# Kernel optimization log

Hardware: AMD Instinct MI355X
Metric: run time of the kernel (lower is better)

Reference implementation:

```python
import jax, jax.numpy as jnp
import numpy as np
import math

EPS = 1e-6
P_MIN = 1e-3
P_MAX = 10.0
NUM_ITERS = 3
REG = 1.0
K = 64       # num_clusters
D = 128      # cluster_dim
TOKEN = 256  # token_dim
B, N, C = 8, 8192, 512


def _l2norm(t):
    return t / jnp.clip(jnp.linalg.norm(t, axis=-1, keepdims=True), 1e-12)


def _mlp(h, W1, b1, W2, b2):
    # torch Linear: y = h @ W.T + b ; dropout is identity at eval
    return jax.nn.relu(h @ W1.T + b1) @ W2.T + b2


def _log_otp_solver(log_a, log_b, M, num_iters, reg):
    M = M / reg
    u = jnp.zeros_like(log_a)
    v = jnp.zeros_like(log_b)
    for _ in range(num_iters):  # fixed small iteration count
        u = log_a - jax.scipy.special.logsumexp(M + v[:, None, :], axis=2)
        v = log_b - jax.scipy.special.logsumexp(M + u[:, :, None], axis=1)
    return M + u[:, :, None] + v[:, None, :]


def _get_matching_probs(S, dustbin_score, num_iters, reg):
    b, m, n = S.shape
    dust_row = jnp.broadcast_to(dustbin_score, (b, 1, n)).astype(S.dtype)
    S_aug = jnp.concatenate([S, dust_row], axis=1)  # [b, m+1, n]
    norm = -math.log(n + m)
    log_a = jnp.full((m + 1,), norm, dtype=S.dtype).at[-1].add(math.log(n - m))
    log_a = jnp.broadcast_to(log_a, (b, m + 1))
    log_b = jnp.full((b, n), norm, dtype=S.dtype)
    log_P = _log_otp_solver(log_a, log_b, S_aug, num_iters, reg)
    return log_P - norm


def setup_inputs() -> dict:
    key = jax.random.key(0)
    ks = jax.random.split(key, 8)
    x = jax.random.normal(ks[0], (B, N, C), dtype=jnp.float32)

    def lin(k, fin, fout):
        k1, k2 = jax.random.split(k)
        W = 0.02 * jax.random.normal(k1, (fout, fin), dtype=jnp.float32)
        b = 0.02 * jax.random.normal(k2, (fout,), dtype=jnp.float32)
        return W, b

    tW1, tb1 = lin(ks[1], C, 512)
    tW2, tb2 = lin(ks[2], 512, TOKEN)
    cW1, cb1 = lin(ks[3], C, 512)
    cW2, cb2 = lin(ks[4], 512, D)
    sW1, sb1 = lin(ks[5], C, 512)
    sW2, sb2 = lin(ks[6], 512, K)
    # GeM p param init so that softplus(w)+p_min == 3.0
    gem_w = jnp.array([math.log(math.exp(3.0 - P_MIN) - 1.0)], dtype=jnp.float32)
    dust_bin = jnp.array(1.0, dtype=jnp.float32)
    return dict(x=x, gem_w=gem_w, dust_bin=dust_bin,
                tW1=tW1, tb1=tb1, tW2=tW2, tb2=tb2,
                cW1=cW1, cb1=cb1, cW2=cW2, cb2=cb2,
                sW1=sW1, sb1=sb1, sW2=sW2, sb2=sb2)


def reference(x, gem_w, dust_bin,
              tW1, tb1, tW2, tb2,
              cW1, cb1, cW2, cb2,
              sW1, sb1, sW2, sb2):
    # --- GeM pooling: [B, N, C] -> [B, C] ---
    p = jnp.minimum(jax.nn.softplus(gem_w) + P_MIN, P_MAX)  # [1]
    g = jnp.mean(jnp.clip(x.astype(jnp.float32), EPS, None) ** p, axis=1) ** (1.0 / p)
    g = jnp.where(jnp.isfinite(g), g, jnp.zeros_like(g))

    global_token = _mlp(g, tW1, tb1, tW2, tb2)          # [B, TOKEN]
    local = _mlp(x, cW1, cb1, cW2, cb2)                 # [B, N, D]
    scores = _mlp(x, sW1, sb1, sW2, sb2)                # [B, N, K]

    S = scores.transpose(0, 2, 1)                       # [B, K, N]
    log_P = _get_matching_probs(S, dust_bin, NUM_ITERS, REG)  # [B, K+1, N]
    p_mat = jnp.exp(log_P)[:, :-1, :]                   # drop dustbin -> [B, K, N]

    # aggregated[b, d, k] = sum_n local[b, n, d] * p[b, k, n]  (no O(B*D*K*N) blowup)
    agg = jnp.einsum('bnd,bkn->bdk', local, p_mat).reshape(x.shape[0], -1)  # [B, D*K]

    result = jnp.concatenate([_l2norm(global_token), _l2norm(agg)], axis=-1)
    return _l2norm(result)
```

## Files before the change

kernel.cpp:

```cpp
#include <hip/hip_runtime.h>
#include <hip/hip_bf16.h>
#include <math.h>

#define BB   8
#define NN   8192
#define CC   512
#define DD   128
#define KK   64
#define TOK  256
#define MM   (BB*NN)

typedef unsigned short u16;
typedef __attribute__((ext_vector_type(8))) short short8;
typedef __attribute__((ext_vector_type(4))) float floatx4;

struct PtrSz { const void* p[15]; int sz[15]; };

__device__ __forceinline__ float bf2f(u16 v) {
    union { unsigned u; float f; } x; x.u = ((unsigned)v) << 16; return x.f;
}
__device__ __forceinline__ u16 f2bf(float f) {
    union { float f; unsigned u; } x; x.f = f;
    unsigned r = x.u + 0x7fffu + ((x.u >> 16) & 1u);
    return (u16)(r >> 16);
}
__device__ __forceinline__ float nat_exp2(float a) {
    float r; asm("v_exp_f32 %0, %1" : "=v"(r) : "v"(a)); return r;
}
__device__ __forceinline__ float nat_log2(float a) {
    float r; asm("v_log_f32 %0, %1" : "=v"(r) : "v"(a)); return r;
}
__device__ __forceinline__ void gload16(const void* g, void* l) {
    __builtin_amdgcn_global_load_lds(
        (const __attribute__((address_space(1))) void*)g,
        (__attribute__((address_space(3))) void*)l, 16, 0, 0);
}

__global__ __launch_bounds__(256)
void fill_sentinel(float* __restrict__ out, int n, float val) {
    int i = blockIdx.x*256 + threadIdx.x;
    if (i < n) out[i] = val;
}

__global__ __launch_bounds__(256)
void detect_all(PtrSz ps, int* __restrict__ flags) {
    int i = blockIdx.x;
    const u16* q = (const u16*)ps.p[i];
    int m = ps.sz[i] < 4096 ? ps.sz[i] : 4096;
    __shared__ int cnt;
    if (threadIdx.x == 0) cnt = 0;
    __syncthreads();
    int c = 0;
    for (int j = threadIdx.x; j < m; j += 256) {
        int e = (q[j] >> 7) & 0xFF;
        if (e < 90 || e > 165) c++;
    }
    atomicAdd(&cnt, c);
    __syncthreads();
    if (threadIdx.x == 0) flags[i] = (cnt * 8 > m) ? 1 : 0;
}

#define W_TW1 0
#define W_TB1 262144
#define W_TW2 262656
#define W_TB2 393728
#define W_CW1 393984
#define W_CB1 656128
#define W_CW2 656640
#define W_CB2 722176
#define W_SW1 722304
#define W_SB1 984448
#define W_SW2 984960
#define W_SB2 1017728
#define W_TOTAL 1017792

__global__ __launch_bounds__(256)
void conv_weights(PtrSz ps, const int* __restrict__ flags,
                  u16* __restrict__ wbuf, float* __restrict__ wscal) {
    long gid = (long)blockIdx.x*256 + threadIdx.x;
    if (gid == 0) {
        float vb = bf2f(((const u16*)ps.p[1])[0]);
        float vf = ((const float*)ps.p[1])[0];
        wscal[0] = (fabsf(vb - 2.94694f) < 0.2f) ? vb : vf;
    } else if (gid == 1) {
        float vb = bf2f(((const u16*)ps.p[2])[0]);
        float vf = ((const float*)ps.p[2])[0];
        wscal[1] = (fabsf(vb - 1.0f) < 0.2f) ? vb : vf;
    }
    if (gid >= W_TOTAL) return;
    int idx; long off;
    if      (gid < W_TB1) { idx = 3;  off = W_TW1; }
    else if (gid < W_TW2) { idx = 4;  off = W_TB1; }
    else if (gid < W_TB2) { idx = 5;  off = W_TW2; }
    else if (gid < W_CW1) { idx = 6;  off = W_TB2; }
    else if (gid < W_CB1) { idx = 7;  off = W_CW1; }
    else if (gid < W_CW2) { idx = 8;  off = W_CB1; }
    else if (gid < W_CB2) { idx = 9;  off = W_CW2; }
    else if (gid < W_SW1) { idx = 10; off = W_CB2; }
    else if (gid < W_SB1) { idx = 11; off = W_SW1; }
    else if (gid < W_SW2) { idx = 12; off = W_SB1; }
    else if (gid < W_SB2) { idx = 13; off = W_SW2; }
    else                  { idx = 14; off = W_SB2; }
    long k = gid - off;
    bool f32in = flags[idx] != 0;
    wbuf[gid] = f32in ? f2bf(((const float*)ps.p[idx])[k]) : ((const u16*)ps.p[idx])[k];
}

__global__ __launch_bounds__(256)
void gem_partial(const void* __restrict__ x, const float* __restrict__ wscal,
                 const int* __restrict__ flags, float* __restrict__ gacc) {
    __shared__ float red[4][512];
    int b = blockIdx.x, ny = blockIdx.y;
    int tid  = threadIdx.x;
    int wave = tid >> 6, lane = tid & 63;
    bool f32in = (flags[0] != 0);
    float gw = wscal[0];
    float p  = fminf(log1pf(expf(gw)) + 1e-3f, 10.0f);
    int c0 = lane*8;
    float s[8];
#pragma unroll
    for (int j = 0; j < 8; ++j) s[j] = 0.f;
    size_t base = ((size_t)b*NN + (size_t)ny*64 + wave)*CC + c0;
    if (f32in) {
        const float* xf = (const float*)x;
#pragma unroll 4
        for (int n = 0; n < 64; n += 4) {
            const float* pf = xf + base + (size_t)n*CC;
            float4 x0 = *(const float4*)pf;
            float4 x1 = *(const float4*)(pf + 4);
            float xv[8] = {x0.x,x0.y,x0.z,x0.w,x1.x,x1.y,x1.z,x1.w};
#pragma unroll
            for (int j = 0; j < 8; ++j)
                s[j] += nat_exp2(p * nat_log2(fmaxf(xv[j], 1e-6f)));
        }
    } else {
        const u16* xu = (const u16*)x;
#pragma unroll 4
        for (int n = 0; n < 64; n += 4) {
            short8 v8 = *(const short8*)(xu + base + (size_t)n*CC);
#pragma unroll
            for (int j = 0; j < 8; ++j)
                s[j] += nat_exp2(p * nat_log2(fmaxf(bf2f((u16)v8[j]), 1e-6f)));
        }
    }
#pragma unroll
    for (int j = 0; j < 8; ++j) red[wave][c0 + j] = s[j];
    __syncthreads();
#pragma unroll
    for (int t = 0; t < 2; ++t) {
        int c = tid + t*256;
        float v = red[0][c] + red[1][c] + red[2][c] + red[3][c];
        atomicAdd(&gacc[b*CC + c], v);
    }
}

__global__ __launch_bounds__(256)
void gem_finalize(const float* __restrict__ gacc, const float* __restrict__ wscal,
                  float* __restrict__ g) {
    int i = blockIdx.x*256 + threadIdx.x;
    float gw = wscal[0];
    float p  = fminf(log1pf(expf(gw)) + 1e-3f, 10.0f);
    float m  = gacc[i] / (float)NN;
    float r  = powf(m, 1.0f/p);
    if (!isfinite(r)) r = 0.f;
    g[i] = r;
}

__global__ __launch_bounds__(512)
void token_mlp(const float* __restrict__ g, const u16* __restrict__ wbuf,
               float* __restrict__ t) {
    __shared__ float gs[CC];
    __shared__ float hs[512];
    int b = blockIdx.x, j = threadIdx.x;
    gs[j] = g[b*CC + j];
    __syncthreads();
    float a = bf2f(wbuf[W_TB1 + j]);
    const u16* w = wbuf + W_TW1 + (size_t)j*CC;
    for (int c = 0; c < CC; ++c) a += gs[c]*bf2f(w[c]);
    hs[j] = fmaxf(a, 0.f);
    __syncthreads();
    if (j < TOK) {
        float a2 = bf2f(wbuf[W_TB2 + j]);
        const u16* w2 = wbuf + W_TW2 + (size_t)j*512;
        for (int c = 0; c < 512; ++c) a2 += hs[c]*bf2f(w2[c]);
        t[b*TOK + j] = a2;
    }
}

template<int BN, int MODE, bool RELU, bool ARAW>
__global__ __launch_bounds__(256)
void gemm_bt(const void* __restrict__ A, const u16* __restrict__ W,
             const u16* __restrict__ bias, void* __restrict__ Cout,
             const int* __restrict__ flags, int N, int Ksz, int lda,
             size_t a_base, int bidx_ovr,
             const u16* __restrict__ W_alt, const u16* __restrict__ bias_alt,
             int nsplit) {
    constexpr int WSUB_N = BN/32;
    constexpr int ATILE = 128*32;
    constexpr int BTILE = BN*32;
    extern __shared__ char smem[];
    u16* a0 = (u16*)smem;
    u16* b0 = a0 + ATILE;
    u16* a1 = b0 + BTILE;
    u16* b1 = a1 + ATILE;
    const int tid  = threadIdx.x;
    const int wave = tid >> 6, lane = tid & 63;
    const int wm = wave >> 1, wn = wave & 1;

    int bx = blockIdx.x, by = blockIdx.y;
    {
        int nbx = gridDim.x, nby = gridDim.y;
        int nwg = nbx*nby;
        if ((nwg & 7) == 0) {
            int lid = bx + by*nbx;
            int q = nwg >> 3;
            int t = (lid & 7)*q + (lid >> 3);
            by = t % nby;
            bx = t / nby;
        }
    }
    const u16* Wp = W; const u16* bp = bias;
    int byw = by;
    if (W_alt != nullptr && by >= nsplit) { Wp = W_alt; bp = bias_alt; byw = by - nsplit; }
    const int bm0 = bx * 128;
    const int bn0 = by * BN;
    const int bw0 = byw * BN;
    const int fr = lane & 15;
    const int fk = (lane >> 4) * 8;
    const bool f32in = ARAW && (flags[0] != 0);

    floatx4 acc[4][WSUB_N];
#pragma unroll
    for (int i = 0; i < 4; ++i)
#pragma unroll
        for (int j = 0; j < WSUB_N; ++j) acc[i][j] = (floatx4){0.f,0.f,0.f,0.f};

    auto STAGE = [&](u16* ab, u16* bb, int k0) {
#pragma unroll
        for (int part = 0; part < 2; ++part) {
            int cb = part*256 + wave*64;
            int mych = cb + lane;
            int row = mych >> 2, kc = (mych & 3)*8;
            gload16((const u16*)A + a_base + (size_t)(bm0 + row)*lda + k0 + kc,
                    ab + (size_t)cb*8);
        }
#pragma unroll
        for (int part = 0; part < BN/64; ++part) {
            int cb = part*256 + wave*64;
            int mych = cb + lane;
            int row = mych >> 2, kc = (mych & 3)*8;
            gload16(Wp + (size_t)(bw0 + row)*Ksz + k0 + kc,
                    bb + (size_t)cb*8);
        }
    };
    auto COMPUTE = [&](const u16* ab, const u16* bb) {
        short8 af[4], bfr[WSUB_N];
#pragma unroll
        for (int i = 0; i < 4; ++i)
            af[i] = *(const short8*)(ab + (wm*64 + i*16 + fr)*32 + fk);
#pragma unroll
        for (int j = 0; j < WSUB_N; ++j)
            bfr[j] = *(const short8*)(bb + (wn*WSUB_N*16 + j*16 + fr)*32 + fk);
#pragma unroll
        for (int i = 0; i < 4; ++i)
#pragma unroll
            for (int j = 0; j < WSUB_N; ++j)
                acc[i][j] = __builtin_amdgcn_mfma_f32_16x16x32_bf16(af[i], bfr[j], acc[i][j], 0, 0, 0);
    };

    if (!f32in) {
        STAGE(a0, b0, 0);
        __syncthreads();
        for (int k0 = 0; k0 < Ksz; k0 += 64) {
            if (k0 + 32 < Ksz) STAGE(a1, b1, k0 + 32);
            COMPUTE(a0, b0);
            __syncthreads();
            if (k0 + 64 < Ksz) STAGE(a0, b0, k0 + 64);
            COMPUTE(a1, b1);
            __syncthreads();
        }
    } else {
        for (int k0 = 0; k0 < Ksz; k0 += 32) {
#pragma unroll
            for (int part = 0; part < 2; ++part) {
                int chunk = part*256 + tid;
                int row = chunk >> 2, kc = (chunk & 3)*8;
                size_t gidx = a_base + (size_t)(bm0 + row)*lda + k0 + kc;
                const float* pf = (const float*)A + gidx;
                float4 x0 = *(const float4*)pf;
                float4 x1 = *(const float4*)(pf + 4);
                short8 vA;
                vA[0]=(short)f2bf(x0.x); vA[1]=(short)f2bf(x0.y);
                vA[2]=(short)f2bf(x0.z); vA[3]=(short)f2bf(x0.w);
                vA[4]=(short)f2bf(x1.x); vA[5]=(short)f2bf(x1.y);
                vA[6]=(short)f2bf(x1.z); vA[7]=(short)f2bf(x1.w);
                *(short8*)(a0 + row*32 + kc) = vA;
            }
#pragma unroll
            for (int part = 0; part < BN/64; ++part) {
                int cb = part*256 + wave*64;
                int mych = cb + lane;
                int row = mych >> 2, kc = (mych & 3)*8;
                gload16(Wp + (size_t)(bw0 + row)*Ksz + k0 + kc,
                        b0 + (size_t)cb*8);
            }
            __syncthreads();
            COMPUTE(a0, b0);
            __syncthreads();
        }
    }

    if constexpr (MODE == 0) {
        u16* cs = (u16*)smem;
#pragma unroll
        for (int i = 0; i < 4; ++i) {
            int row0 = wm*64 + i*16 + ((lane>>4)<<2);
#pragma unroll
            for (int j = 0; j < WSUB_N; ++j) {
                int col = wn*WSUB_N*16 + j*16 + fr;
                float bb = bf2f(bp[bw0+col]);
#pragma unroll
                for (int r = 0; r < 4; ++r) {
                    float v = acc[i][j][r] + bb;
                    if (RELU) v = fmaxf(v, 0.f);
                    cs[(row0+r)*BN + col] = f2bf(v);
                }
            }
        }
        __syncthreads();
        u16* C = (u16*)Cout;
#pragma unroll
        for (int c = 0; c < (128*BN)/(256*8); ++c) {
            int flat = (c*256 + tid)*8;
            int rowt = flat / BN, colt = flat % BN;
            *(short8*)(C + (size_t)(bm0+rowt)*N + bn0 + colt) =
                *(const short8*)(cs + flat);
        }
    } else {
        const int bidx = (bidx_ovr >= 0) ? bidx_ovr : (bm0 >> 13);
        const int nin  = bm0 & 8191;
        if constexpr (MODE == 1) {
            u16* tr = (u16*)smem;
#pragma unroll
            for (int i = 0; i < 4; ++i) {
                int row0 = wm*64 + i*16 + ((lane>>4)<<2);
#pragma unroll
                for (int j = 0; j < WSUB_N; ++j) {
                    int col = wn*WSUB_N*16 + j*16 + fr;
                    float bb = bf2f(bp[bw0+col]);
#pragma unroll
                    for (int r = 0; r < 4; ++r) {
                        float v = acc[i][j][r] + bb;
                        if (RELU) v = fmaxf(v, 0.f);
                        tr[col*128 + row0 + r] = f2bf(v);
                    }
                }
            }
            __syncthreads();
            u16* O = (u16*)Cout;
#pragma unroll
            for (int c = 0; c < (BN*128)/256; ++c) {
                int flat = c*256 + tid;
                int dcol = flat >> 7, rr = flat & 127;
                O[(size_t)(bidx*BN + bn0 + dcol)*NN + nin + rr] = tr[dcol*128 + rr];
            }
        } else {
            float* tr = (float*)smem;
#pragma unroll
            for (int i = 0; i < 4; ++i) {
                int row0 = wm*64 + i*16 + ((lane>>4)<<2);
#pragma unroll
                for (int j = 0; j < WSUB_N; ++j) {
                    int col = wn*WSUB_N*16 + j*16 + fr;
                    float bb = bf2f(bp[bw0+col]);
#pragma unroll
                    for (int r = 0; r < 4; ++r) {
                        float v = acc[i][j][r] + bb;
                        if (RELU) v = fmaxf(v, 0.f);
                        tr[col*128 + row0 + r] = v;
                    }
                }
            }
            __syncthreads();
            float* O = (float*)Cout;
#pragma unroll
            for (int c = 0; c < (BN*128)/256; ++c) {
                int flat = c*256 + tid;
                int dcol = flat >> 7, rr = flat & 127;
                O[(size_t)(bidx*BN + bn0 + dcol)*NN + nin + rr] = tr[dcol*128 + rr];
            }
        }
    }
}

__global__ __launch_bounds__(256)
void sink_u(const float* __restrict__ ST, const float* __restrict__ v,
            const float* __restrict__ wscal, float* __restrict__ u) {
    int m = blockIdx.x, b = blockIdx.y, t = threadIdx.x;
    const float norm = -logf(8256.0f);
    float la = (m == 64) ? norm + logf(8128.0f) : norm;
    float dustf = wscal[1];
    const float* vb = v + (size_t)b*NN;
    float r[32];
    float mx = -1e30f;
    if (m < 64) {
        const float* row = ST + ((size_t)b*64 + m)*NN;
#pragma unroll
        for (int i = 0; i < 32; ++i) { int n = t + i*256; r[i] = row[n] + vb[n]; mx = fmaxf(mx, r[i]); }
    } else {
#pragma unroll
        for (int i = 0; i < 32; ++i) { int n = t + i*256; r[i] = dustf + vb[n]; mx = fmaxf(mx, r[i]); }
    }
#pragma unroll
    for (int off = 32; off; off >>= 1) mx = fmaxf(mx, __shfl_xor(mx, off));
    __shared__ float red[4];
    if ((t & 63) == 0) red[t>>6] = mx;
    __syncthreads();
    mx = fmaxf(fmaxf(red[0], red[1]), fmaxf(red[2], red[3]));
    __syncthreads();
    float s = 0.f;
#pragma unroll
    for (int i = 0; i < 32; ++i) s += expf(r[i] - mx);
#pragma unroll
    for (int off = 32; off; off >>= 1) s += __shfl_xor(s, off);
    if ((t & 63) == 0) red[t>>6] = s;
    __syncthreads();
    s = red[0] + red[1] + red[2] + red[3];
    if (t == 0) u[b*65 + m] = la - (mx + logf(s));
}

template<int WP>
__global__ __launch_bounds__(256)
void sink_v_t(const float* __restrict__ ST, const float* __restrict__ u,
              const float* __restrict__ wscal, float* __restrict__ v,
              u16* __restrict__ P) {
    int b = blockIdx.y;
    int n = blockIdx.x*256 + threadIdx.x;
    __shared__ float us[65];
    if (threadIdx.x < 65) us[threadIdx.x] = u[b*65 + threadIdx.x];
    __syncthreads();
    const float norm = -logf(8256.0f);
    float mx = wscal[1] + us[64];
    float s  = 1.0f;
    const float* col = ST + (size_t)b*64*NN + n;
    if (WP) {
        float r[64];
#pragma unroll
        for (int m = 0; m < 64; ++m) {
            r[m] = col[(size_t)m*NN] + us[m];
            float nm = fmaxf(mx, r[m]);
            s = s*expf(mx - nm) + expf(r[m] - nm);
            mx = nm;
        }
        float vn = norm - (mx + logf(s));
        v[(size_t)b*NN + n] = vn;
#pragma unroll
        for (int k = 0; k < 64; ++k)
            P[((size_t)b*64 + k)*NN + n] = f2bf(expf(r[k] + vn - norm));
    } else {
        for (int m = 0; m < 64; ++m) {
            float tv = col[(size_t)m*NN] + us[m];
            float nm = fmaxf(mx, tv);
            s = s*expf(mx - nm) + expf(tv - nm);
            mx = nm;
        }
        v[(size_t)b*NN + n] = norm - (mx + logf(s));
    }
}

__global__ __launch_bounds__(256)
void agg_mfma(const u16* __restrict__ localT, const u16* __restrict__ P,
              float* __restrict__ agg) {
    __shared__ u16 a_lds[128*32];
    __shared__ u16 b_lds[64*32];
    int b = blockIdx.y, ns = blockIdx.x;
    int n0 = ns*256;
    const int tid  = threadIdx.x;
    const int wave = tid >> 6, lane = tid & 63;
    const int wm = wave >> 1, wn = wave & 1;
    const int fr = lane & 15, fk = (lane >> 4)*8;

    floatx4 acc[4][2];
#pragma unroll
    for (int i = 0; i < 4; ++i)
#pragma unroll
        for (int j = 0; j < 2; ++j) acc[i][j] = (floatx4){0.f,0.f,0.f,0.f};

    for (int s = 0; s < 8; ++s) {
        int nk = n0 + s*32;
#pragma unroll
        for (int part = 0; part < 2; ++part) {
            int chunk = part*256 + tid;
            int row = chunk >> 2, kc = (chunk & 3)*8;
            short8 vA = *(const short8*)(localT + ((size_t)b*128 + row)*NN + nk + kc);
            *(short8*)(a_lds + row*32 + kc) = vA;
        }
        {
            int row = tid >> 2, kc = (tid & 3)*8;
            short8 vB = *(const short8*)(P + ((size_t)b*64 + row)*NN + nk + kc);
            *(short8*)(b_lds + row*32 + kc) = vB;
        }
        __syncthreads();
        short8 af[4], bfr[2];
#pragma unroll
        for (int i = 0; i < 4; ++i)
            af[i] = *(const short8*)(a_lds + (wm*64 + i*16 + fr)*32 + fk);
#pragma unroll
        for (int j = 0; j < 2; ++j)
            bfr[j] = *(const short8*)(b_lds + (wn*32 + j*16 + fr)*32 + fk);
#pragma unroll
        for (int i = 0; i < 4; ++i)
#pragma unroll
            for (int j = 0; j < 2; ++j)
                acc[i][j] = __builtin_amdgcn_mfma_f32_16x16x32_bf16(af[i], bfr[j], acc[i][j], 0, 0, 0);
        __syncthreads();
    }
#pragma unroll
    for (int i = 0; i < 4; ++i) {
        int d0 = wm*64 + i*16 + ((lane>>4)<<2);
#pragma unroll
        for (int j = 0; j < 2; ++j) {
            int k = wn*32 + j*16 + fr;
#pragma unroll
            for (int r = 0; r < 4; ++r)
                atomicAdd(&agg[(size_t)b*8192 + (d0+r)*64 + k], acc[i][j][r]);
        }
    }
}

__global__ __launch_bounds__(256)
void finalize_out(const float* __restrict__ tg, const float* __restrict__ agg,
                  float* __restrict__ out) {
    int b = blockIdx.x, tid = threadIdx.x;
    float tv = tg[b*TOK + tid];
    float s1 = tv*tv;
    const float* ab = agg + (size_t)b*8192;
    float av[32];
    float s2 = 0.f;
#pragma unroll
    for (int i = 0; i < 32; ++i) { av[i] = ab[tid + i*256]; s2 += av[i]*av[i]; }
#pragma unroll
    for (int off = 32; off; off >>= 1) { s1 += __shfl_xor(s1, off); s2 += __shfl_xor(s2, off); }
    __shared__ float r1[4], r2[4];
    int wave = tid >> 6, lane = tid & 63;
    if (lane == 0) { r1[wave] = s1; r2[wave] = s2; }
    __syncthreads();
    float S1 = r1[0]+r1[1]+r1[2]+r1[3];
    float S2 = r2[0]+r2[1]+r2[2]+r2[3];
    const float rs2 = 1.41421356237f;
    float sc1 = 1.0f/(fmaxf(sqrtf(S1), 1e-12f)*rs2);
    float sc2 = 1.0f/(fmaxf(sqrtf(S2), 1e-12f)*rs2);
    out[(size_t)b*8448 + tid] = tv*sc1;
#pragma unroll
    for (int i = 0; i < 32; ++i)
        out[(size_t)b*8448 + 256 + tid + i*256] = av[i]*sc2;
}

extern "C" void kernel_launch(void* const* d_in, const int* in_sizes, int n_in,
                              void* d_out, int out_size, void* d_ws, size_t ws_size,
                              hipStream_t stream) {
    float* out = (float*)d_out;

    static const int EXP[15] = {33554432,1,1,262144,512,131072,256,
                                262144,512,65536,128,262144,512,32768,64};
    bool ok = (n_in == 15) && (out_size == 67584);
    if (ok) for (int i = 0; i < 15; ++i) ok = ok && (in_sizes[i] == EXP[i]);
    if (!ok) {
        fill_sentinel<<<264, 256, 0, stream>>>(out, out_size, 0.25f);
        return;
    }
    const size_t NEED_BATCH = 52934656ull;
    if (ws_size < NEED_BATCH) {
        fill_sentinel<<<264, 256, 0, stream>>>(out, out_size, 0.5f);
        return;
    }

    const void* x = d_in[0];
    PtrSz ps;
    for (int i = 0; i < 15; ++i) { ps.p[i] = d_in[i]; ps.sz[i] = in_sizes[i]; }

    char* base = (char*)d_ws;
    float* gacc = (float*)(base + 0);
    float* u    = (float*)(base + 16384);
    float* v    = (float*)(base + 18464);
    float* agg  = (float*)(base + 280608);
    const size_t ZERO_BYTES = 542752;
    float* g    = (float*)(base + 542752);
    float* tglb = (float*)(base + 559136);
    int*   flags= (int*)  (base + 567328);
    float* wscal= (float*)(base + 567392);
    u16*   wbuf = (u16*)  (base + 567424);
    float* ST   = (float*)(base + 2603008);
    u16* localT = (u16*)  (base + 19380224);
    u16* P      = (u16*)  (base + 36157440);
    u16* h1     = (u16*)  (base + 44546048);
    const size_t FULL_NEED  = 44546048ull + 67108864ull;
    const size_t FUSED_NEED = 44546048ull + 134217728ull;
    const bool fused = (ws_size >= FUSED_NEED);
    const bool mono  = (ws_size >= FULL_NEED);

    hipMemsetAsync(d_ws, 0, ZERO_BYTES, stream);

    detect_all<<<15, 256, 0, stream>>>(ps, flags);
    conv_weights<<<3977, 256, 0, stream>>>(ps, flags, wbuf, wscal);

    gem_partial<<<dim3(BB, 128), 256, 0, stream>>>(x, wscal, flags, gacc);
    gem_finalize<<<16, 256, 0, stream>>>(gacc, wscal, g);
    token_mlp<<<BB, 512, 0, stream>>>(g, wbuf, tglb);

    const int NOSPLIT = 1 << 30;
    if (fused) {
        gemm_bt<128, 0, true,  true ><<<dim3(512, 8), 256, 32768, stream>>>(
            x, wbuf + W_CW1, wbuf + W_CB1, h1, flags, 1024, 512, 512, 0, -1,
            wbuf + W_SW1, wbuf + W_SB1, 4);
        gemm_bt<128, 1, false, false><<<dim3(512, 1), 256, 32768, stream>>>(
            h1, wbuf + W_CW2, wbuf + W_CB2, localT, flags, 128, 512, 1024, 0, -1,
            nullptr, nullptr, NOSPLIT);
        gemm_bt< 64, 2, false, false><<<dim3(512, 1), 256, 32768, stream>>>(
            h1, wbuf + W_SW2, wbuf + W_SB2, ST, flags, 64, 512, 1024, 512, -1,
            nullptr, nullptr, NOSPLIT);
    } else if (mono) {
        gemm_bt<128, 0, true,  true ><<<dim3(512, 4), 256, 32768, stream>>>(
            x, wbuf + W_CW1, wbuf + W_CB1, h1, flags, 512, 512, 512, 0, -1,
            nullptr, nullptr, NOSPLIT);
        gemm_bt<128, 1, false, false><<<dim3(512, 1), 256, 32768, stream>>>(
            h1, wbuf + W_CW2, wbuf + W_CB2, localT, flags, 128, 512, 512, 0, -1,
            nullptr, nullptr, NOSPLIT);
        gemm_bt<128, 0, true,  true ><<<dim3(512, 4), 256, 32768, stream>>>(
            x, wbuf + W_SW1, wbuf + W_SB1, h1, flags, 512, 512, 512, 0, -1,
            nullptr, nullptr, NOSPLIT);
        gemm_bt< 64, 2, false, false><<<dim3(512, 1), 256, 32768, stream>>>(
            h1, wbuf + W_SW2, wbuf + W_SB2, ST, flags, 64, 512, 512, 0, -1,
            nullptr, nullptr, NOSPLIT);
    } else {
        for (int b = 0; b < BB; ++b) {
            size_t ab = (size_t)b*NN*CC;
            gemm_bt<128, 0, true,  true ><<<dim3(64, 4), 256, 32768, stream>>>(
                x, wbuf + W_CW1, wbuf + W_CB1, h1, flags, 512, 512, 512, ab, -1,
                nullptr, nullptr, NOSPLIT);
            gemm_bt<128, 1, false, false><<<dim3(64, 1), 256, 32768, stream>>>(
                h1, wbuf + W_CW2, wbuf + W_CB2, localT, flags, 128, 512, 512, 0, b,
                nullptr, nullptr, NOSPLIT);
            gemm_bt<128, 0, true,  true ><<<dim3(64, 4), 256, 32768, stream>>>(
                x, wbuf + W_SW1, wbuf + W_SB1, h1, flags, 512, 512, 512, ab, -1,
                nullptr, nullptr, NOSPLIT);
            gemm_bt< 64, 2, false, false><<<dim3(64, 1), 256, 32768, stream>>>(
                h1, wbuf + W_SW2, wbuf + W_SB2, ST, flags, 64, 512, 512, 0, b,
                nullptr, nullptr, NOSPLIT);
        }
    }

    for (int it = 0; it < 3; ++it) {
        sink_u<<<dim3(65, BB), 256, 0, stream>>>(ST, v, wscal, u);
        if (it == 2)
            sink_v_t<1><<<dim3(32, BB), 256, 0, stream>>>(ST, u, wscal, v, P);
        else
            sink_v_t<0><<<dim3(32, BB), 256, 0, stream>>>(ST, u, wscal, v, P);
    }

    agg_mfma<<<dim3(32, BB), 256, 0, stream>>>(localT, P, agg);
    finalize_out<<<BB, 256, 0, stream>>>(tglb, agg, out);
}
```

Measured before the change: 547.1 us.

## Drop GEMM LDS double buffering and write MODE 0 output directly to global

Replaces the double-buffered LDS staging loop in gemm_bt with a single-buffered load/sync/compute/sync loop. The MODE 0 epilogue now writes scalar bf16 values straight to global memory instead of staging through LDS for vectorized 16-byte stores. The first-layer GEMM launches drop their dynamic shared memory request from 32 KB to 16 KB, which may allow more workgroups per CU. In exchange it loses the overlap of global loads with MFMA compute and replaces coalesced wide stores with scattered 2-byte writes.

```diff
diff --git a/kernel.cpp b/kernel.cpp
--- a/kernel.cpp
+++ b/kernel.cpp
@@ -196,13 +196,9 @@
              const u16* __restrict__ W_alt, const u16* __restrict__ bias_alt,
              int nsplit) {
     constexpr int WSUB_N = BN/32;
-    constexpr int ATILE = 128*32;
-    constexpr int BTILE = BN*32;
     extern __shared__ char smem[];
-    u16* a0 = (u16*)smem;
-    u16* b0 = a0 + ATILE;
-    u16* a1 = b0 + BTILE;
-    u16* b1 = a1 + ATILE;
+    u16* a_lds = (u16*)smem;
+    u16* b_lds = (u16*)smem + 128*32;
     const int tid  = threadIdx.x;
     const int wave = tid >> 6, lane = tid & 63;
     const int wm = wave >> 1, wn = wave & 1;
@@ -235,52 +231,8 @@
 #pragma unroll
         for (int j = 0; j < WSUB_N; ++j) acc[i][j] = (floatx4){0.f,0.f,0.f,0.f};
 
-    auto STAGE = [&](u16* ab, u16* bb, int k0) {
-#pragma unroll
-        for (int part = 0; part < 2; ++part) {
-            int cb = part*256 + wave*64;
-            int mych = cb + lane;
-            int row = mych >> 2, kc = (mych & 3)*8;
-            gload16((const u16*)A + a_base + (size_t)(bm0 + row)*lda + k0 + kc,
-                    ab + (size_t)cb*8);
-        }
-#pragma unroll
-        for (int part = 0; part < BN/64; ++part) {
-            int cb = part*256 + wave*64;
-            int mych = cb + lane;
-            int row = mych >> 2, kc = (mych & 3)*8;
-            gload16(Wp + (size_t)(bw0 + row)*Ksz + k0 + kc,
-                    bb + (size_t)cb*8);
-        }
-    };
-    auto COMPUTE = [&](const u16* ab, const u16* bb) {
-        short8 af[4], bfr[WSUB_N];
-#pragma unroll
-        for (int i = 0; i < 4; ++i)
-            af[i] = *(const short8*)(ab + (wm*64 + i*16 + fr)*32 + fk);
-#pragma unroll
-        for (int j = 0; j < WSUB_N; ++j)
-            bfr[j] = *(const short8*)(bb + (wn*WSUB_N*16 + j*16 + fr)*32 + fk);
-#pragma unroll
-        for (int i = 0; i < 4; ++i)
-#pragma unroll
-            for (int j = 0; j < WSUB_N; ++j)
-                acc[i][j] = __builtin_amdgcn_mfma_f32_16x16x32_bf16(af[i], bfr[j], acc[i][j], 0, 0, 0);
-    };
-
-    if (!f32in) {
-        STAGE(a0, b0, 0);
-        __syncthreads();
-        for (int k0 = 0; k0 < Ksz; k0 += 64) {
-            if (k0 + 32 < Ksz) STAGE(a1, b1, k0 + 32);
-            COMPUTE(a0, b0);
-            __syncthreads();
-            if (k0 + 64 < Ksz) STAGE(a0, b0, k0 + 64);
-            COMPUTE(a1, b1);
-            __syncthreads();
-        }
-    } else {
-        for (int k0 = 0; k0 < Ksz; k0 += 32) {
+    for (int k0 = 0; k0 < Ksz; k0 += 32) {
+        if (f32in) {
 #pragma unroll
             for (int part = 0; part < 2; ++part) {
                 int chunk = part*256 + tid;
@@ -294,24 +246,44 @@
                 vA[2]=(short)f2bf(x0.z); vA[3]=(short)f2bf(x0.w);
                 vA[4]=(short)f2bf(x1.x); vA[5]=(short)f2bf(x1.y);
                 vA[6]=(short)f2bf(x1.z); vA[7]=(short)f2bf(x1.w);
-                *(short8*)(a0 + row*32 + kc) = vA;
+                *(short8*)(a_lds + row*32 + kc) = vA;
             }
-#pragma unroll
-            for (int part = 0; part < BN/64; ++part) {
+        } else {
+#pragma unroll
+            for (int part = 0; part < 2; ++part) {
                 int cb = part*256 + wave*64;
                 int mych = cb + lane;
                 int row = mych >> 2, kc = (mych & 3)*8;
-                gload16(Wp + (size_t)(bw0 + row)*Ksz + k0 + kc,
-                        b0 + (size_t)cb*8);
+                gload16((const u16*)A + a_base + (size_t)(bm0 + row)*lda + k0 + kc,
+                        a_lds + (size_t)cb*8);
             }
-            __syncthreads();
-            COMPUTE(a0, b0);
-            __syncthreads();
-        }
+        }
+#pragma unroll
+        for (int part = 0; part < BN/64; ++part) {
+            int cb = part*256 + wave*64;
+            int mych = cb + lane;
+            int row = mych >> 2, kc = (mych & 3)*8;
+            gload16(Wp + (size_t)(bw0 + row)*Ksz + k0 + kc,
+                    b_lds + (size_t)cb*8);
+        }
+        __syncthreads();
+        short8 af[4], bfr[WSUB_N];
+#pragma unroll
+        for (int i = 0; i < 4; ++i)
+            af[i] = *(const short8*)(a_lds + (wm*64 + i*16 + fr)*32 + fk);
+#pragma unroll
+        for (int j = 0; j < WSUB_N; ++j)
+            bfr[j] = *(const short8*)(b_lds + (wn*WSUB_N*16 + j*16 + fr)*32 + fk);
+#pragma unroll
+        for (int i = 0; i < 4; ++i)
+#pragma unroll
+            for (int j = 0; j < WSUB_N; ++j)
+                acc[i][j] = __builtin_amdgcn_mfma_f32_16x16x32_bf16(af[i], bfr[j], acc[i][j], 0, 0, 0);
+        __syncthreads();
     }
 
     if constexpr (MODE == 0) {
-        u16* cs = (u16*)smem;
+        u16* C = (u16*)Cout;
 #pragma unroll
         for (int i = 0; i < 4; ++i) {
             int row0 = wm*64 + i*16 + ((lane>>4)<<2);
@@ -323,18 +295,9 @@
                 for (int r = 0; r < 4; ++r) {
                     float v = acc[i][j][r] + bb;
                     if (RELU) v = fmaxf(v, 0.f);
-                    cs[(row0+r)*BN + col] = f2bf(v);
+                    C[(size_t)(bm0+row0+r)*N + (bn0+col)] = f2bf(v);
                 }
             }
-        }
-        __syncthreads();
-        u16* C = (u16*)Cout;
-#pragma unroll
-        for (int c = 0; c < (128*BN)/(256*8); ++c) {
-            int flat = (c*256 + tid)*8;
-            int rowt = flat / BN, colt = flat % BN;
-            *(short8*)(C + (size_t)(bm0+rowt)*N + bn0 + colt) =
-                *(const short8*)(cs + flat);
         }
     } else {
         const int bidx = (bidx_ovr >= 0) ? bidx_ovr : (bm0 >> 13);
@@ -610,7 +573,7 @@
 
     const int NOSPLIT = 1 << 30;
     if (fused) {
-        gemm_bt<128, 0, true,  true ><<<dim3(512, 8), 256, 32768, stream>>>(
+        gemm_bt<128, 0, true,  true ><<<dim3(512, 8), 256, 16384, stream>>>(
             x, wbuf + W_CW1, wbuf + W_CB1, h1, flags, 1024, 512, 512, 0, -1,
             wbuf + W_SW1, wbuf + W_SB1, 4);
         gemm_bt<128, 1, false, false><<<dim3(512, 1), 256, 32768, stream>>>(
@@ -620,13 +583,13 @@
             h1, wbuf + W_SW2, wbuf + W_SB2, ST, flags, 64, 512, 1024, 512, -1,
             nullptr, nullptr, NOSPLIT);
     } else if (mono) {
-        gemm_bt<128, 0, true,  true ><<<dim3(512, 4), 256, 32768, stream>>>(
+        gemm_bt<128, 0, true,  true ><<<dim3(512, 4), 256, 16384, stream>>>(
             x, wbuf + W_CW1, wbuf + W_CB1, h1, flags, 512, 512, 512, 0, -1,
             nullptr, nullptr, NOSPLIT);
         gemm_bt<128, 1, false, false><<<dim3(512, 1), 256, 32768, stream>>>(
             h1, wbuf + W_CW2, wbuf + W_CB2, localT, flags, 128, 512, 512, 0, -1,
             nullptr, nullptr, NOSPLIT);
-        gemm_bt<128, 0, true,  true ><<<dim3(512, 4), 256, 32768, stream>>>(
+        gemm_bt<128, 0, true,  true ><<<dim3(512, 4), 256, 16384, stream>>>(
             x, wbuf + W_SW1, wbuf + W_SB1, h1, flags, 512, 512, 512, 0, -1,
             nullptr, nullptr, NOSPLIT);
         gemm_bt< 64, 2, false, false><<<dim3(512, 1), 256, 32768, stream>>>(
@@ -635,13 +598,13 @@
     } else {
         for (int b = 0; b < BB; ++b) {
             size_t ab = (size_t)b*NN*CC;
-            gemm_bt<128, 0, true,  true ><<<dim3(64, 4), 256, 32768, stream>>>(
+            gemm_bt<128, 0, true,  true ><<<dim3(64, 4), 256, 16384, stream>>>(
                 x, wbuf + W_CW1, wbuf + W_CB1, h1, flags, 512, 512, 512, ab, -1,
                 nullptr, nullptr, NOSPLIT);
             gemm_bt<128, 1, false, false><<<dim3(64, 1), 256, 32768, stream>>>(
                 h1, wbuf + W_CW2, wbuf + W_CB2, localT, flags, 128, 512, 512, 0, b,
                 nullptr, nullptr, NOSPLIT);
-            gemm_bt<128, 0, true,  true ><<<dim3(64, 4), 256, 32768, stream>>>(
+            gemm_bt<128, 0, true,  true ><<<dim3(64, 4), 256, 16384, stream>>>(
                 x, wbuf + W_SW1, wbuf + W_SB1, h1, flags, 512, 512, 512, ab, -1,
                 nullptr, nullptr, NOSPLIT);
             gemm_bt< 64, 2, false, false><<<dim3(64, 1), 256, 32768, stream>>>(
```

Measured after the change: 514.3 us. 6.0% less time.
